# Kernel tuning notes

Measured on AMD Instinct MI355X. Metric: run time of the kernel, lower is better.

Reference implementation:

```python
import jax, jax.numpy as jnp
import numpy as np
from functools import partial

B, N, D = 32, 256, 1024
H = 16
HD = D // H
CD = 1024          # cond_dim
E = 4              # num_experts
TOPK = 2
DFF = 4 * D        # expert hidden
RH = 2 * D         # router mlp hidden
TEMP = 1.0
EPS = 1e-5


def _ln(x, g, b):
    mu = jnp.mean(x, axis=-1, keepdims=True)
    var = jnp.var(x, axis=-1, keepdims=True)
    return (x - mu) * jax.lax.rsqrt(var + EPS) * g + b


def setup_inputs() -> dict:
    key = jax.random.key(0)
    ks = jax.random.split(key, 16)
    s = 0.02
    return {
        "x": jax.random.normal(ks[0], (B, N, D), jnp.float32),
        "cond": jax.random.normal(ks[1], (B, 1, CD), jnp.float32),
        "ln1_g": jnp.ones((D,), jnp.float32),
        "ln1_b": jnp.zeros((D,), jnp.float32),
        "qkv_w": jax.random.normal(ks[2], (D, 3 * D), jnp.float32) * s,
        "proj_w": jax.random.normal(ks[3], (D, D), jnp.float32) * s,
        "proj_b": jnp.zeros((D,), jnp.float32),
        "ln2_g": jnp.ones((D,), jnp.float32),
        "ln2_b": jnp.zeros((D,), jnp.float32),
        "r_fc1_w": jax.random.normal(ks[4], (D + CD, RH), jnp.float32) * s,
        "r_fc1_b": jnp.zeros((RH,), jnp.float32),
        "r_fc2_w": jax.random.normal(ks[5], (RH, E), jnp.float32) * s,
        "r_fc2_b": jnp.zeros((E,), jnp.float32),
        "e_w1": jax.random.normal(ks[6], (E, D, DFF), jnp.float32) * s,
        "e_b1": jnp.zeros((E, DFF), jnp.float32),
        "e_w2": jax.random.normal(ks[7], (E, DFF, D), jnp.float32) * s,
        "e_b2": jnp.zeros((E, D), jnp.float32),
    }


def reference(x, cond, ln1_g, ln1_b, qkv_w, proj_w, proj_b, ln2_g, ln2_b,
              r_fc1_w, r_fc1_b, r_fc2_w, r_fc2_b, e_w1, e_b1, e_w2, e_b2):
    gelu = partial(jax.nn.gelu, approximate=False)  # torch nn.GELU default (erf)

    # ---- Attention block (pre-LN, no mask, qkv_bias=False) ----
    h = _ln(x, ln1_g, ln1_b)
    qkv = (h @ qkv_w).reshape(B, N, 3, H, HD)
    q, k, v = jnp.moveaxis(qkv, 2, 0)                         # each [B,N,H,HD]
    scale = HD ** -0.5
    attn = jnp.einsum("bqhd,bkhd->bhqk", q * scale, k)        # [B,H,N,N]
    attn = jax.nn.softmax(attn, axis=-1)
    o = jnp.einsum("bhqk,bkhd->bqhd", attn, v).reshape(B, N, D)
    x = x + o @ proj_w + proj_b

    # ---- RouterCond: concat tokens with repeated cond, MLP -> expert logits ----
    h = _ln(x, ln2_g, ln2_b)
    cond_rep = jnp.broadcast_to(cond, (B, N, CD))             # repeat along seq
    rin = jnp.concatenate([h, cond_rep], axis=-1).reshape(-1, D + CD)  # [T, D+CD]
    logits = gelu(rin @ r_fc1_w + r_fc1_b) @ r_fc2_w + r_fc2_b         # [T, E]
    logits = (logits - jnp.max(logits, axis=-1, keepdims=True)) / TEMP
    probs = jnp.clip(jax.nn.softmax(logits, axis=-1), 1e-9, 1.0 - 1e-9)

    # top-k selection + renormalization, scatter to dense router mask [T, E]
    top_p, top_i = jax.lax.top_k(probs, TOPK)
    top_w = top_p / jnp.sum(top_p, axis=-1, keepdims=True)    # normalize=True
    T = B * N
    router_mask = jnp.zeros((T, E), probs.dtype).at[
        jnp.arange(T)[:, None], top_i].set(top_w)             # [T, E]

    # ---- Expert MLPs, combined by router weights ----
    hf = h.reshape(T, D)
    hid = gelu(jnp.einsum("td,edh->teh", hf, e_w1) + e_b1)    # [T, E, DFF]
    eout = jnp.einsum("teh,ehd->ted", hid, e_w2) + e_b2       # [T, E, D]
    moe = jnp.einsum("te,ted->td", router_mask, eout).reshape(B, N, D)

    return x + moe
```

## Files before the change

### kernel.cpp

```cpp
#include <hip/hip_runtime.h>


typedef unsigned short u16;
typedef unsigned int   u32;

typedef __bf16 bf16x8 __attribute__((ext_vector_type(8)));
typedef float  floatx4 __attribute__((ext_vector_type(4)));

__device__ __forceinline__ float b2f(u32 u) {
    union { float f; u32 i; } v; v.i = (u & 0xffffu) << 16; return v.f;
}
__device__ __forceinline__ u16 f2b(float f) {
    union { float f; u32 i; } v; v.f = f;
    u32 x = v.i;
    u32 r = (x + 0x7fffu + ((x >> 16) & 1u)) >> 16;
    return (u16)r;
}
__device__ __forceinline__ float gelu_f(float x) {
    return 0.5f * x * (1.0f + erff(x * 0.70710678118654752440f));
}
__device__ __forceinline__ float lmix(const void* p, size_t i, int isf) {
    return isf ? ((const float*)p)[i] : b2f(((const u16*)p)[i]);
}
__device__ __forceinline__ void ld8(const void* p, size_t i, int isf, float w[8]) {
    if (isf) {
        const float* q = (const float*)p + i;
        float4 a = *(const float4*)q, b = *(const float4*)(q + 4);
        w[0] = a.x; w[1] = a.y; w[2] = a.z; w[3] = a.w;
        w[4] = b.x; w[5] = b.y; w[6] = b.z; w[7] = b.w;
    } else {
        const u16* q = (const u16*)p + i;
        uint4 r = *(const uint4*)q;
        w[0] = b2f(r.x); w[1] = b2f(r.x >> 16);
        w[2] = b2f(r.y); w[3] = b2f(r.y >> 16);
        w[4] = b2f(r.z); w[5] = b2f(r.z >> 16);
        w[6] = b2f(r.w); w[7] = b2f(r.w >> 16);
    }
}
__device__ __forceinline__ void ld4(const void* p, size_t i, int isf, float w[4]) {
    if (isf) {
        float4 a = *(const float4*)((const float*)p + i);
        w[0] = a.x; w[1] = a.y; w[2] = a.z; w[3] = a.w;
    } else {
        uint2 r = *(const uint2*)((const u16*)p + i);
        w[0] = b2f(r.x); w[1] = b2f(r.x >> 16);
        w[2] = b2f(r.y); w[3] = b2f(r.y >> 16);
    }
}

__global__ void init_kernel(const void* x0, int* cb) {
    __shared__ int sh[256];
    const int tid = threadIdx.x;
    if (tid < 12) cb[tid] = 0;
    int bad = 0;
    const u16* p = (const u16*)x0;
    for (int i = tid; i < 4096; i += 256) {
        float v = b2f(p[2 * i]);
        float a = fabsf(v);
        if (!(a <= 1e3f) || (v != 0.f && a < 1e-8f)) bad++;
    }
    sh[tid] = bad;
    __syncthreads();
    for (int s = 128; s > 0; s >>= 1) {
        if (tid < s) sh[tid] += sh[tid + s];
        __syncthreads();
    }
    if (tid == 0) cb[12] = (sh[0] > 512) ? 1 : 0;
}

__global__ __launch_bounds__(256) void cond_kernel(
    const void* __restrict__ cond, const void* __restrict__ w1,
    float* __restrict__ ct, const int* __restrict__ flg)
{
    const int isf = flg[12];
    const int b = blockIdx.y;
    const int col0 = blockIdx.x * 64;
    const int tid = threadIdx.x;
    const int wave = tid >> 6, lane = tid & 63;
    __shared__ float a[1024];
    __shared__ float part[4][64];
    {
        float v[4];
        ld4(cond, (size_t)b * 1024 + tid * 4, isf, v);
        a[tid * 4 + 0] = v[0]; a[tid * 4 + 1] = v[1];
        a[tid * 4 + 2] = v[2]; a[tid * 4 + 3] = v[3];
    }
    __syncthreads();
    const int col = col0 + lane;
    float s = 0.f;
    const int kbase = wave * 256;
    #pragma unroll 4
    for (int k = 0; k < 256; k++)
        s = fmaf(a[kbase + k], lmix(w1, (size_t)(1024 + kbase + k) * 2048 + col, isf), s);
    part[wave][lane] = s;
    __syncthreads();
    if (wave == 0) {
        float r = (part[0][lane] + part[1][lane]) + (part[2][lane] + part[3][lane]);
        ct[(size_t)b * 2048 + col] = r;
    }
}

__global__ __launch_bounds__(256) void pack_ln_kernel(
    int mode, const void* __restrict__ xin, size_t rowbase,
    const void* __restrict__ g, const void* __restrict__ bta,
    const float* __restrict__ mu_g, const float* __restrict__ rs_g,
    u16* __restrict__ hpk, u16* __restrict__ hb, const int* __restrict__ flg)
{
    const int isf = flg[12];
    const int row = blockIdx.x, tid = threadIdx.x;
    float v[4];
    float mu, rsv;
    __shared__ float red[8];
    __shared__ float mu_rs[2];
    if (mode == 0) {
        ld4(xin, (rowbase + row) * 1024 + tid * 4, isf, v);
        float s = v[0] + v[1] + v[2] + v[3];
        float q = v[0] * v[0] + v[1] * v[1] + v[2] * v[2] + v[3] * v[3];
        #pragma unroll
        for (int off = 32; off > 0; off >>= 1) {
            s += __shfl_down(s, off, 64);
            q += __shfl_down(q, off, 64);
        }
        int wid = tid >> 6, lane = tid & 63;
        if (lane == 0) { red[wid] = s; red[4 + wid] = q; }
        __syncthreads();
        if (tid == 0) {
            float ts = red[0] + red[1] + red[2] + red[3];
            float tq = red[4] + red[5] + red[6] + red[7];
            float m = ts * (1.0f / 1024.0f);
            float var = tq * (1.0f / 1024.0f) - m * m;
            float xx = var + 1e-5f;
            float r = rsqrtf(xx);
            r = r * (1.5f - 0.5f * xx * r * r);
            mu_rs[0] = m; mu_rs[1] = r;
        }
        __syncthreads();
        mu = mu_rs[0]; rsv = mu_rs[1];
    } else {
        float4 t = *(const float4*)((const float*)xin + (rowbase + row) * 1024 + tid * 4);
        v[0] = t.x; v[1] = t.y; v[2] = t.z; v[3] = t.w;
        mu = mu_g[rowbase + row]; rsv = rs_g[rowbase + row];
    }
    float gg[4], bb[4];
    ld4(g, tid * 4, isf, gg);
    ld4(bta, tid * 4, isf, bb);
    u16 hi[4], lo[4];
    #pragma unroll
    for (int i = 0; i < 4; i++) {
        float h = (v[i] - mu) * rsv * gg[i] + bb[i];
        hi[i] = f2b(h);
        lo[i] = f2b(h - b2f(hi[i]));
    }
    uint2 ph, pl;
    ph.x = (u32)hi[0] | ((u32)hi[1] << 16);
    ph.y = (u32)hi[2] | ((u32)hi[3] << 16);
    pl.x = (u32)lo[0] | ((u32)lo[1] << 16);
    pl.y = (u32)lo[2] | ((u32)lo[3] << 16);
    *(uint2*)(hpk + (size_t)row * 2048 + tid * 4) = ph;
    *(uint2*)(hpk + (size_t)row * 2048 + 1024 + tid * 4) = pl;
    if (hb) *(uint2*)(hb + (rowbase + row) * 1024 + tid * 4) = ph;
}

__global__ __launch_bounds__(256) void pack_wt_kernel(
    const void* __restrict__ W, int N, int K,
    u16* __restrict__ Bt, const int* __restrict__ flg)
{
    const int isf = flg[12];
    __shared__ float sh[64][65];
    const int k0 = blockIdx.x * 64, n0 = blockIdx.y * 64;
    const int tid = threadIdx.x;
    #pragma unroll
    for (int i = 0; i < 4; i++) {
        int r = (tid >> 4) + i * 16, c = (tid & 15) * 4;
        float w[4];
        ld4(W, (size_t)(k0 + r) * N + n0 + c, isf, w);
        sh[r][c] = w[0]; sh[r][c + 1] = w[1]; sh[r][c + 2] = w[2]; sh[r][c + 3] = w[3];
    }
    __syncthreads();
    const int n = tid >> 2, kc = (tid & 3) * 16;
    u16 hi[16], lo[16];
    #pragma unroll
    for (int j = 0; j < 16; j++) {
        float v = sh[kc + j][n];
        hi[j] = f2b(v);
        lo[j] = f2b(v - b2f(hi[j]));
    }
    u16* dst = Bt + (size_t)(n0 + n) * (2 * K) + k0 + kc;
    uint4 a, b;
    a.x = (u32)hi[0] | ((u32)hi[1] << 16);  a.y = (u32)hi[2] | ((u32)hi[3] << 16);
    a.z = (u32)hi[4] | ((u32)hi[5] << 16);  a.w = (u32)hi[6] | ((u32)hi[7] << 16);
    b.x = (u32)hi[8] | ((u32)hi[9] << 16);  b.y = (u32)hi[10] | ((u32)hi[11] << 16);
    b.z = (u32)hi[12] | ((u32)hi[13] << 16); b.w = (u32)hi[14] | ((u32)hi[15] << 16);
    *(uint4*)dst = a; *(uint4*)(dst + 8) = b;
    a.x = (u32)lo[0] | ((u32)lo[1] << 16);  a.y = (u32)lo[2] | ((u32)lo[3] << 16);
    a.z = (u32)lo[4] | ((u32)lo[5] << 16);  a.w = (u32)lo[6] | ((u32)lo[7] << 16);
    b.x = (u32)lo[8] | ((u32)lo[9] << 16);  b.y = (u32)lo[10] | ((u32)lo[11] << 16);
    b.z = (u32)lo[12] | ((u32)lo[13] << 16); b.w = (u32)lo[14] | ((u32)lo[15] << 16);
    *(uint4*)(dst + K) = a; *(uint4*)(dst + K + 8) = b;
}

__global__ __launch_bounds__(256) void pack_wtb_kernel(
    const void* __restrict__ W, size_t wOff, int N, int K,
    u16* __restrict__ Bt, const int* __restrict__ flg)
{
    const int isf = flg[12];
    __shared__ float sh[64][65];
    const int k0 = blockIdx.x * 64, n0 = blockIdx.y * 64;
    const int tid = threadIdx.x;
    #pragma unroll
    for (int i = 0; i < 4; i++) {
        int r = (tid >> 4) + i * 16, c = (tid & 15) * 4;
        float w[4];
        ld4(W, wOff + (size_t)(k0 + r) * N + n0 + c, isf, w);
        sh[r][c] = w[0]; sh[r][c + 1] = w[1]; sh[r][c + 2] = w[2]; sh[r][c + 3] = w[3];
    }
    __syncthreads();
    const int n = tid >> 2, kc = (tid & 3) * 16;
    u16 hi[16];
    #pragma unroll
    for (int j = 0; j < 16; j++) hi[j] = f2b(sh[kc + j][n]);
    u16* dst = Bt + (size_t)(n0 + n) * K + k0 + kc;
    uint4 a, b;
    a.x = (u32)hi[0] | ((u32)hi[1] << 16);  a.y = (u32)hi[2] | ((u32)hi[3] << 16);
    a.z = (u32)hi[4] | ((u32)hi[5] << 16);  a.w = (u32)hi[6] | ((u32)hi[7] << 16);
    b.x = (u32)hi[8] | ((u32)hi[9] << 16);  b.y = (u32)hi[10] | ((u32)hi[11] << 16);
    b.z = (u32)hi[12] | ((u32)hi[13] << 16); b.w = (u32)hi[14] | ((u32)hi[15] << 16);
    *(uint4*)dst = a; *(uint4*)(dst + 8) = b;
}

__global__ __launch_bounds__(256) void pack_sb_rows_kernel(
    const float* __restrict__ src, u16* __restrict__ dst)
{
    const int row = blockIdx.x, tid = threadIdx.x;
    float4 t = *(const float4*)(src + (size_t)row * 1024 + tid * 4);
    float v[4] = {t.x, t.y, t.z, t.w};
    u16 hi[4], lo[4];
    #pragma unroll
    for (int i = 0; i < 4; i++) {
        hi[i] = f2b(v[i]);
        lo[i] = f2b(v[i] - b2f(hi[i]));
    }
    uint2 ph, pl;
    ph.x = (u32)hi[0] | ((u32)hi[1] << 16);
    ph.y = (u32)hi[2] | ((u32)hi[3] << 16);
    pl.x = (u32)lo[0] | ((u32)lo[1] << 16);
    pl.y = (u32)lo[2] | ((u32)lo[3] << 16);
    *(uint2*)(dst + (size_t)row * 2048 + tid * 4) = ph;
    *(uint2*)(dst + (size_t)row * 2048 + 1024 + tid * 4) = pl;
}

#define SB_PLAIN 0
#define SB_FC1   1
#define SB_PROJ  2

__global__ __launch_bounds__(256) void gemm_sb(
    int mode,
    const u16* __restrict__ Ap,
    const u16* __restrict__ Bt,
    int K,
    float* __restrict__ C, int ldc,
    const void* __restrict__ bias,
    const float* __restrict__ condt,
    const void* __restrict__ resid,
    int rowbase, const int* __restrict__ flg)
{
    const int isf = flg[12];
    __shared__ __align__(16) u16 Ah[128][40];
    __shared__ __align__(16) u16 Al[128][40];
    __shared__ __align__(16) u16 Bh[128][40];
    __shared__ __align__(16) u16 Bl[128][40];
    const int tid = threadIdx.x;
    const int row0 = blockIdx.y * 128, col0 = blockIdx.x * 128;
    const int wave = tid >> 6, lane = tid & 63;
    const int wm = (wave >> 1) * 64, wn = (wave & 1) * 64;
    const int ln = lane & 15, quad = lane >> 4;
    const size_t K2 = (size_t)2 * K;
    floatx4 acc[4][4];
    #pragma unroll
    for (int i = 0; i < 4; i++)
        #pragma unroll
        for (int j = 0; j < 4; j++) acc[i][j] = (floatx4){0.f, 0.f, 0.f, 0.f};

    const int ar = tid >> 1, ac = (tid & 1) * 16;
    uint4 pa0, pa1, pal0, pal1, pb0, pb1, pbl0, pbl1;

    {
        const u16* ap = Ap + (size_t)(row0 + ar) * K2 + ac;
        pa0 = *(const uint4*)ap;        pa1 = *(const uint4*)(ap + 8);
        pal0 = *(const uint4*)(ap + K); pal1 = *(const uint4*)(ap + K + 8);
        const u16* bp = Bt + (size_t)(col0 + ar) * K2 + ac;
        pb0 = *(const uint4*)bp;        pb1 = *(const uint4*)(bp + 8);
        pbl0 = *(const uint4*)(bp + K); pbl1 = *(const uint4*)(bp + K + 8);
    }

    for (int k0 = 0; k0 < K; k0 += 32) {
        __syncthreads();
        *(uint4*)&Ah[ar][ac] = pa0;  *(uint4*)&Ah[ar][ac + 8] = pa1;
        *(uint4*)&Al[ar][ac] = pal0; *(uint4*)&Al[ar][ac + 8] = pal1;
        *(uint4*)&Bh[ar][ac] = pb0;  *(uint4*)&Bh[ar][ac + 8] = pb1;
        *(uint4*)&Bl[ar][ac] = pbl0; *(uint4*)&Bl[ar][ac + 8] = pbl1;
        __syncthreads();
        if (k0 + 32 < K) {
            const u16* ap = Ap + (size_t)(row0 + ar) * K2 + k0 + 32 + ac;
            pa0 = *(const uint4*)ap;        pa1 = *(const uint4*)(ap + 8);
            pal0 = *(const uint4*)(ap + K); pal1 = *(const uint4*)(ap + K + 8);
            const u16* bp = Bt + (size_t)(col0 + ar) * K2 + k0 + 32 + ac;
            pb0 = *(const uint4*)bp;        pb1 = *(const uint4*)(bp + 8);
            pbl0 = *(const uint4*)(bp + K); pbl1 = *(const uint4*)(bp + K + 8);
        }
        bf16x8 ah[4], al[4];
        #pragma unroll
        for (int mt = 0; mt < 4; mt++) {
            ah[mt] = *(const bf16x8*)&Ah[wm + mt * 16 + ln][quad * 8];
            al[mt] = *(const bf16x8*)&Al[wm + mt * 16 + ln][quad * 8];
        }
        #pragma unroll
        for (int nt = 0; nt < 4; nt++) {
            bf16x8 bh = *(const bf16x8*)&Bh[wn + nt * 16 + ln][quad * 8];
            bf16x8 bl = *(const bf16x8*)&Bl[wn + nt * 16 + ln][quad * 8];
            #pragma unroll
            for (int mt = 0; mt < 4; mt++) {
                acc[mt][nt] = __builtin_amdgcn_mfma_f32_16x16x32_bf16(ah[mt], bh, acc[mt][nt], 0, 0, 0);
                acc[mt][nt] = __builtin_amdgcn_mfma_f32_16x16x32_bf16(ah[mt], bl, acc[mt][nt], 0, 0, 0);
                acc[mt][nt] = __builtin_amdgcn_mfma_f32_16x16x32_bf16(al[mt], bh, acc[mt][nt], 0, 0, 0);
            }
        }
    }
    #pragma unroll
    for (int mt = 0; mt < 4; mt++) {
        #pragma unroll
        for (int nt = 0; nt < 4; nt++) {
            #pragma unroll
            for (int r = 0; r < 4; r++) {
                int row = row0 + wm + mt * 16 + quad * 4 + r;
                int col = col0 + wn + nt * 16 + ln;
                float v = acc[mt][nt][r];
                if (mode == SB_FC1)
                    v = gelu_f(v + lmix(bias, col, isf) +
                               condt[(size_t)((rowbase + row) >> 8) * 2048 + col]);
                else if (mode == SB_PROJ)
                    v += lmix(bias, col, isf) + lmix(resid, (size_t)row * ldc + col, isf);
                C[(size_t)row * ldc + col] = v;
            }
        }
    }
}

#define MOE_FC1 0
#define MOE_FC2 1

__global__ __launch_bounds__(256) void gemm_moe(
    int mode,
    const u16* __restrict__ Ap,
    const u16* __restrict__ Bt,
    int K,
    u16* __restrict__ C, int ldc,
    const void* __restrict__ bias, size_t biasOff,
    const float* __restrict__ rowscale,
    const int* __restrict__ toklist,
    const int* __restrict__ cb, int e, int rowOff,
    const int* __restrict__ flg)
{
    const int isf = flg[12];
    const int Meff = cb[e];
    const int gbase = cb[4 + e];
    const int rg0 = rowOff + blockIdx.y * 128;
    if (rg0 >= Meff) return;
    const int col0 = blockIdx.x * 128;
    __shared__ __align__(16) u16 As[128][40];
    __shared__ __align__(16) u16 Bs[128][40];
    const int tid = threadIdx.x;
    const int wave = tid >> 6, lane = tid & 63;
    const int wm = (wave >> 1) * 64, wn = (wave & 1) * 64;
    const int ln = lane & 15, quad = lane >> 4;
    floatx4 acc[4][4];
    #pragma unroll
    for (int i = 0; i < 4; i++)
        #pragma unroll
        for (int j = 0; j < 4; j++) acc[i][j] = (floatx4){0.f, 0.f, 0.f, 0.f};

    const int ar = tid >> 1, ac = (tid & 1) * 16;
    const int rg = rg0 + ar;
    const bool valid = (rg < Meff);
    const u16* arow;
    if (mode == MOE_FC1) {
        int tokid = valid ? toklist[gbase + rg] : 0;
        arow = Ap + (size_t)tokid * K;
    } else {
        arow = Ap + (size_t)(rg - rowOff) * K;
    }
    const u16* brow = Bt + (size_t)(col0 + ar) * K;
    uint4 pa0 = {0u,0u,0u,0u}, pa1 = {0u,0u,0u,0u}, pb0, pb1;
    if (valid) { pa0 = *(const uint4*)(arow + ac); pa1 = *(const uint4*)(arow + ac + 8); }
    pb0 = *(const uint4*)(brow + ac); pb1 = *(const uint4*)(brow + ac + 8);

    for (int k0 = 0; k0 < K; k0 += 32) {
        __syncthreads();
        *(uint4*)&As[ar][ac] = pa0; *(uint4*)&As[ar][ac + 8] = pa1;
        *(uint4*)&Bs[ar][ac] = pb0; *(uint4*)&Bs[ar][ac + 8] = pb1;
        __syncthreads();
        if (k0 + 32 < K) {
            if (valid) {
                pa0 = *(const uint4*)(arow + k0 + 32 + ac);
                pa1 = *(const uint4*)(arow + k0 + 32 + ac + 8);
            }
            pb0 = *(const uint4*)(brow + k0 + 32 + ac);
            pb1 = *(const uint4*)(brow + k0 + 32 + ac + 8);
        }
        bf16x8 a[4];
        #pragma unroll
        for (int mt = 0; mt < 4; mt++)
            a[mt] = *(const bf16x8*)&As[wm + mt * 16 + ln][quad * 8];
        #pragma unroll
        for (int nt = 0; nt < 4; nt++) {
            bf16x8 b = *(const bf16x8*)&Bs[wn + nt * 16 + ln][quad * 8];
            #pragma unroll
            for (int mt = 0; mt < 4; mt++)
                acc[mt][nt] = __builtin_amdgcn_mfma_f32_16x16x32_bf16(a[mt], b, acc[mt][nt], 0, 0, 0);
        }
    }
    #pragma unroll
    for (int mt = 0; mt < 4; mt++) {
        #pragma unroll
        for (int nt = 0; nt < 4; nt++) {
            #pragma unroll
            for (int r = 0; r < 4; r++) {
                int gw = rg0 + wm + mt * 16 + quad * 4 + r;
                if (gw >= Meff) continue;
                int col = col0 + wn + nt * 16 + ln;
                float v = acc[mt][nt][r] + lmix(bias, biasOff + col, isf);
                if (mode == MOE_FC1) {
                    C[(size_t)(gw - rowOff) * ldc + col] = f2b(gelu_f(v));
                } else {
                    v *= rowscale[gbase + gw];
                    C[(size_t)(gbase + gw) * ldc + col] = f2b(v);
                }
            }
        }
    }
}

__global__ __launch_bounds__(256) void gemm_moe2(
    const u16* __restrict__ Ap,
    const u16* __restrict__ Bt,
    u16* __restrict__ C,
    const void* __restrict__ bias, size_t biasOff,
    const float* __restrict__ rowscale,
    const int* __restrict__ cb, int e, int rowOff,
    const int* __restrict__ flg)
{
    const int isf = flg[12];
    const int Meff = cb[e];
    const int gbase = cb[4 + e];
    const int rg0 = rowOff + blockIdx.y * 128;
    if (rg0 >= Meff) return;
    const int col0 = blockIdx.x * 64;
    const int K = 4096;
    __shared__ __align__(16) u16 As[128][40];
    __shared__ __align__(16) u16 Bs[64][40];
    const int tid = threadIdx.x;
    const int wave = tid >> 6, lane = tid & 63;
    const int ln = lane & 15, quad = lane >> 4;
    floatx4 acc[2][4];
    #pragma unroll
    for (int i = 0; i < 2; i++)
        #pragma unroll
        for (int j = 0; j < 4; j++) acc[i][j] = (floatx4){0.f, 0.f, 0.f, 0.f};

    const int ar = tid >> 1, ac = (tid & 1) * 16;
    const int br = tid >> 2, bc = (tid & 3) * 8;
    const int rg = rg0 + ar;
    const bool valid = (rg < Meff);
    const u16* arow = Ap + (size_t)(rg - rowOff) * K;
    const u16* brow = Bt + (size_t)(col0 + br) * K;
    uint4 pa0 = {0u,0u,0u,0u}, pa1 = {0u,0u,0u,0u}, pb;
    if (valid) { pa0 = *(const uint4*)(arow + ac); pa1 = *(const uint4*)(arow + ac + 8); }
    pb = *(const uint4*)(brow + bc);

    for (int k0 = 0; k0 < K; k0 += 32) {
        __syncthreads();
        *(uint4*)&As[ar][ac] = pa0; *(uint4*)&As[ar][ac + 8] = pa1;
        *(uint4*)&Bs[br][bc] = pb;
        __syncthreads();
        if (k0 + 32 < K) {
            if (valid) {
                pa0 = *(const uint4*)(arow + k0 + 32 + ac);
                pa1 = *(const uint4*)(arow + k0 + 32 + ac + 8);
            }
            pb = *(const uint4*)(brow + k0 + 32 + bc);
        }
        bf16x8 a0 = *(const bf16x8*)&As[wave * 32 + ln][quad * 8];
        bf16x8 a1 = *(const bf16x8*)&As[wave * 32 + 16 + ln][quad * 8];
        #pragma unroll
        for (int nt = 0; nt < 4; nt++) {
            bf16x8 b = *(const bf16x8*)&Bs[nt * 16 + ln][quad * 8];
            acc[0][nt] = __builtin_amdgcn_mfma_f32_16x16x32_bf16(a0, b, acc[0][nt], 0, 0, 0);
            acc[1][nt] = __builtin_amdgcn_mfma_f32_16x16x32_bf16(a1, b, acc[1][nt], 0, 0, 0);
        }
    }
    #pragma unroll
    for (int mt = 0; mt < 2; mt++) {
        #pragma unroll
        for (int nt = 0; nt < 4; nt++) {
            #pragma unroll
            for (int r = 0; r < 4; r++) {
                int gw = rg0 + wave * 32 + mt * 16 + quad * 4 + r;
                if (gw >= Meff) continue;
                int col = col0 + nt * 16 + ln;
                float v = acc[mt][nt][r] + lmix(bias, biasOff + col, isf);
                v *= rowscale[gbase + gw];
                C[(size_t)(gbase + gw) * 1024 + col] = f2b(v);
            }
        }
    }
}

__global__ __launch_bounds__(256) void ln_stats_kernel(
    const float* __restrict__ xin, float* __restrict__ mu, float* __restrict__ rs)
{
    const int row = blockIdx.x, tid = threadIdx.x;
    float4 t = *(const float4*)(xin + (size_t)row * 1024 + tid * 4);
    float s = t.x + t.y + t.z + t.w;
    float q = t.x * t.x + t.y * t.y + t.z * t.z + t.w * t.w;
    #pragma unroll
    for (int off = 32; off > 0; off >>= 1) {
        s += __shfl_down(s, off, 64);
        q += __shfl_down(q, off, 64);
    }
    __shared__ float red[8];
    int wid = tid >> 6, lane = tid & 63;
    if (lane == 0) { red[wid] = s; red[4 + wid] = q; }
    __syncthreads();
    if (tid == 0) {
        float ts = red[0] + red[1] + red[2] + red[3];
        float tq = red[4] + red[5] + red[6] + red[7];
        float m = ts * (1.0f / 1024.0f);
        float var = tq * (1.0f / 1024.0f) - m * m;
        float xx = var + 1e-5f;
        float r = rsqrtf(xx);
        r = r * (1.5f - 0.5f * xx * r * r);
        mu[row] = m; rs[row] = r;
    }
}

#define GM_PLAIN 0
#define GM_PROJ  1

__global__ __launch_bounds__(256) void gemm_f32(
    int mode, int aMode,
    const void* __restrict__ Av, int lda,
    const void* __restrict__ Bv, int ldb, int bRow0,
    int M, int N, int K,
    float* __restrict__ C, int ldc,
    const void* __restrict__ bias,
    const void* __restrict__ resid,
    const int* __restrict__ flg)
{
    const int isf = flg[12];
    __shared__ float As[16][132];
    __shared__ float Bs[16][132];
    const int tid = threadIdx.x;
    const int row0 = blockIdx.y * 128, col0 = blockIdx.x * 128;
    const int tx = tid & 15, ty = tid >> 4;
    float acc[8][8];
    #pragma unroll
    for (int i = 0; i < 8; i++)
        #pragma unroll
        for (int j = 0; j < 8; j++) acc[i][j] = 0.f;

    for (int k0 = 0; k0 < K; k0 += 16) {
        __syncthreads();
        #pragma unroll
        for (int i = 0; i < 2; i++) {
            int lin = tid + i * 256;
            int r = lin >> 2, kc = (lin & 3) * 4;
            float v[4] = {0.f, 0.f, 0.f, 0.f};
            if (row0 + r < M) {
                if (aMode == 1) {
                    ld4(Av, (size_t)(row0 + r) * lda + k0 + kc, isf, v);
                } else {
                    float4 t = *(const float4*)((const float*)Av + (size_t)(row0 + r) * lda + k0 + kc);
                    v[0] = t.x; v[1] = t.y; v[2] = t.z; v[3] = t.w;
                }
            }
            As[kc + 0][r] = v[0]; As[kc + 1][r] = v[1];
            As[kc + 2][r] = v[2]; As[kc + 3][r] = v[3];
        }
        {
            int kc = tid >> 4, c8 = (tid & 15) * 8;
            float w[8];
            ld8(Bv, (size_t)(bRow0 + k0 + kc) * ldb + col0 + c8, isf, w);
            #pragma unroll
            for (int j = 0; j < 8; j++) Bs[kc][c8 + j] = w[j];
        }
        __syncthreads();
        #pragma unroll
        for (int kk = 0; kk < 16; kk++) {
            float a[8], b[8];
            *(float4*)&a[0] = *(const float4*)&As[kk][ty * 8];
            *(float4*)&a[4] = *(const float4*)&As[kk][ty * 8 + 4];
            *(float4*)&b[0] = *(const float4*)&Bs[kk][tx * 8];
            *(float4*)&b[4] = *(const float4*)&Bs[kk][tx * 8 + 4];
            #pragma unroll
            for (int i = 0; i < 8; i++)
                #pragma unroll
                for (int j = 0; j < 8; j++) acc[i][j] = fmaf(a[i], b[j], acc[i][j]);
        }
    }
    #pragma unroll
    for (int i = 0; i < 8; i++) {
        int gr = row0 + ty * 8 + i;
        if (gr >= M) continue;
        #pragma unroll
        for (int j = 0; j < 8; j++) {
            int gc = col0 + tx * 8 + j;
            float v = acc[i][j];
            if (mode == GM_PROJ)
                v += lmix(bias, gc, isf) + lmix(resid, (size_t)gr * ldc + gc, isf);
            C[(size_t)gr * ldc + gc] = v;
        }
    }
}

__global__ __launch_bounds__(256) void attn_kernel(
    const float* __restrict__ qkv, float* __restrict__ o)
{
    const int bx = blockIdx.x;
    const int b  = bx >> 6;
    const int hh = (bx >> 2) & 15;
    const int qt = bx & 3;
    const int tid = threadIdx.x;
    const int wave = tid >> 6, lane = tid & 63;

    __shared__ float sh[2 * 64 * 68];
    float* Ks = sh;
    float* Vs = sh + 64 * 68;

    const int q = qt * 64 + lane;
    float qreg[64];
    const float* qp = qkv + (size_t)(b * 256 + q) * 3072 + hh * 64;
    #pragma unroll
    for (int i = 0; i < 16; i++) *(float4*)&qreg[i * 4] = *(const float4*)(qp + i * 4);

    float oa[64];
    #pragma unroll
    for (int d = 0; d < 64; d++) oa[d] = 0.f;
    float m = -1e30f, l = 0.f;

    for (int s = 0; s < 4; s++) {
        __syncthreads();
        {
            int r = tid >> 2;
            int c = (tid & 3) * 16;
            int key = (r >> 4) * 64 + s * 16 + (r & 15);
            const float* kp = qkv + (size_t)(b * 256 + key) * 3072 + 1024 + hh * 64 + c;
            #pragma unroll
            for (int i = 0; i < 4; i++) {
                *(float4*)&Ks[r * 68 + c + i * 4] = *(const float4*)(kp + i * 4);
                *(float4*)&Vs[r * 68 + c + i * 4] = *(const float4*)(kp + 1024 + i * 4);
            }
        }
        __syncthreads();
        const float* Kw = Ks + wave * 16 * 68;
        const float* Vw = Vs + wave * 16 * 68;
        for (int jj = 0; jj < 16; jj++) {
            float s0 = 0.f, s1 = 0.f, s2 = 0.f, s3 = 0.f;
            #pragma unroll
            for (int d = 0; d < 64; d += 4) {
                s0 = fmaf(qreg[d + 0], Kw[jj * 68 + d + 0], s0);
                s1 = fmaf(qreg[d + 1], Kw[jj * 68 + d + 1], s1);
                s2 = fmaf(qreg[d + 2], Kw[jj * 68 + d + 2], s2);
                s3 = fmaf(qreg[d + 3], Kw[jj * 68 + d + 3], s3);
            }
            float sc = ((s0 + s1) + (s2 + s3)) * 0.125f;
            float mn = fmaxf(m, sc);
            float c = __expf(m - mn);
            float p = __expf(sc - mn);
            l = l * c + p;
            #pragma unroll
            for (int d = 0; d < 64; d++)
                oa[d] = fmaf(oa[d], c, p * Vw[jj * 68 + d]);
            m = mn;
        }
    }

    __syncthreads();
    if (wave == 1 || wave == 3) {
        float* dst = sh + (wave >> 1) * (64 * 66) + lane * 66;
        #pragma unroll
        for (int d = 0; d < 64; d++) dst[d] = oa[d];
        dst[64] = m; dst[65] = l;
    }
    __syncthreads();
    if (wave == 0 || wave == 2) {
        const float* src = sh + (wave >> 1) * (64 * 66) + lane * 66;
        float m2 = src[64], l2 = src[65];
        float M = fmaxf(m, m2);
        float c1 = __expf(m - M), c2 = __expf(m2 - M);
        l = l * c1 + l2 * c2;
        #pragma unroll
        for (int d = 0; d < 64; d++) oa[d] = oa[d] * c1 + src[d] * c2;
        m = M;
    }
    __syncthreads();
    if (wave == 2) {
        float* dst = sh + lane * 66;
        #pragma unroll
        for (int d = 0; d < 64; d++) dst[d] = oa[d];
        dst[64] = m; dst[65] = l;
    }
    __syncthreads();
    if (wave == 0) {
        const float* src = sh + lane * 66;
        float m2 = src[64], l2 = src[65];
        float M = fmaxf(m, m2);
        float c1 = __expf(m - M), c2 = __expf(m2 - M);
        l = l * c1 + l2 * c2;
        #pragma unroll
        for (int d = 0; d < 64; d++) oa[d] = oa[d] * c1 + src[d] * c2;
        float inv = 1.0f / l;
        float* op = o + (size_t)(b * 256 + q) * 1024 + hh * 64;
        #pragma unroll
        for (int i = 0; i < 16; i++) {
            float4 v = { oa[i * 4] * inv, oa[i * 4 + 1] * inv,
                         oa[i * 4 + 2] * inv, oa[i * 4 + 3] * inv };
            *(float4*)(op + i * 4) = v;
        }
    }
}

__global__ __launch_bounds__(256) void router_kernel(
    const float* __restrict__ hr, const void* __restrict__ w2,
    const void* __restrict__ b2, int* __restrict__ t2i,
    float* __restrict__ t2w, int* __restrict__ cb, int rowbase,
    const int* __restrict__ flg)
{
    const int isf = flg[12];
    const int lt = blockIdx.x * 4 + (threadIdx.x >> 6);
    const int t = rowbase + lt;
    const int lane = threadIdx.x & 63;
    float a0 = 0.f, a1 = 0.f, a2 = 0.f, a3 = 0.f;
    const float* hp = hr + (size_t)lt * 2048;
    for (int j = lane; j < 2048; j += 64) {
        float hv = hp[j];
        float w[4];
        ld4(w2, (size_t)j * 4, isf, w);
        a0 = fmaf(hv, w[0], a0);
        a1 = fmaf(hv, w[1], a1);
        a2 = fmaf(hv, w[2], a2);
        a3 = fmaf(hv, w[3], a3);
    }
    #pragma unroll
    for (int off = 32; off > 0; off >>= 1) {
        a0 += __shfl_down(a0, off, 64);
        a1 += __shfl_down(a1, off, 64);
        a2 += __shfl_down(a2, off, 64);
        a3 += __shfl_down(a3, off, 64);
    }
    if (lane == 0) {
        float l[4];
        l[0] = a0 + lmix(b2, 0, isf); l[1] = a1 + lmix(b2, 1, isf);
        l[2] = a2 + lmix(b2, 2, isf); l[3] = a3 + lmix(b2, 3, isf);
        int i0 = 0;
        #pragma unroll
        for (int i = 1; i < 4; i++) if (l[i] > l[i0]) i0 = i;
        int i1 = (i0 == 0) ? 1 : 0;
        #pragma unroll
        for (int i = 0; i < 4; i++) if (i != i0 && l[i] > l[i1]) i1 = i;
        float mx = fmaxf(fmaxf(l[0], l[1]), fmaxf(l[2], l[3]));
        float e0 = __expf(l[0] - mx), e1 = __expf(l[1] - mx);
        float e2 = __expf(l[2] - mx), e3 = __expf(l[3] - mx);
        float inv = 1.0f / (e0 + e1 + e2 + e3);
        float p[4] = { e0 * inv, e1 * inv, e2 * inv, e3 * inv };
        float b0 = fminf(fmaxf(p[i0], 1e-9f), 1.0f - 1e-9f);
        float b1 = fminf(fmaxf(p[i1], 1e-9f), 1.0f - 1e-9f);
        float winv = 1.0f / (b0 + b1);
        t2i[2 * t] = i0; t2i[2 * t + 1] = i1;
        t2w[2 * t] = b0 * winv; t2w[2 * t + 1] = b1 * winv;
        atomicAdd(&cb[i0], 1);
        atomicAdd(&cb[i1], 1);
    }
}

__global__ __launch_bounds__(256) void fill2_kernel(
    const int* __restrict__ t2i, const float* __restrict__ t2w,
    int* __restrict__ cb, int* __restrict__ tok,
    float* __restrict__ aw, int* __restrict__ apos)
{
    const int e = blockIdx.x;
    const int tid = threadIdx.x;
    __shared__ int scan[256];
    int base = 0;
    #pragma unroll
    for (int i = 0; i < 4; i++) if (i < e) base += cb[i];
    const int t0 = tid * 32;
    int cnt = 0;
    for (int t = t0; t < t0 + 32; t++)
        cnt += (t2i[2 * t] == e) + (t2i[2 * t + 1] == e);
    scan[tid] = cnt;
    __syncthreads();
    for (int off = 1; off < 256; off <<= 1) {
        int add = (tid >= off) ? scan[tid - off] : 0;
        __syncthreads();
        scan[tid] += add;
        __syncthreads();
    }
    int pos = base + scan[tid] - cnt;
    for (int t = t0; t < t0 + 32; t++) {
        #pragma unroll
        for (int j = 0; j < 2; j++) {
            if (t2i[2 * t + j] == e) {
                tok[pos] = t;
                aw[pos] = t2w[2 * t + j];
                apos[2 * t + j] = pos;
                pos++;
            }
        }
    }
    if (tid == 0) cb[4 + e] = base;
}

#define EM_FC1 0
#define EM_FC2 1

__global__ __launch_bounds__(256) void gemm_mfma(
    int mode,
    const float* __restrict__ x1,
    const float* __restrict__ mu, const float* __restrict__ rs,
    const void* __restrict__ lng, const void* __restrict__ lnb,
    const u16* __restrict__ Ab,
    const void* __restrict__ B, size_t bOff, int ldb, int K,
    u16* __restrict__ C, int ldc,
    const void* __restrict__ bias, size_t biasOff,
    const float* __restrict__ rowscale,
    const int* __restrict__ toklist,
    const int* __restrict__ cb, int e, int rowOff,
    const int* __restrict__ flg)
{
    const int isf = flg[12];
    const int Meff = cb[e];
    const int gbase = cb[4 + e];
    const int rg0 = rowOff + blockIdx.y * 64;
    if (rg0 >= Meff) return;
    const int col0 = blockIdx.x * 64;
    __shared__ __align__(16) u16 As[64][72];
    __shared__ __align__(16) u16 Bs[64][72];
    const int tid = threadIdx.x;
    const int wave = tid >> 6, lane = tid & 63;
    const int ln = lane & 15, quad = lane >> 4;
    floatx4 acc[4];
    #pragma unroll
    for (int nt = 0; nt < 4; nt++) acc[nt] = (floatx4){0.f, 0.f, 0.f, 0.f};

    const int ar = tid >> 2, ac = (tid & 3) * 8;
    const int bk = tid >> 3, bn = (tid & 7) * 8;
    const int rg = rg0 + ar;
    const bool valid = (rg < Meff);
    int tokid = 0; float lm = 0.f, lr = 0.f;
    if (mode == EM_FC1 && valid) {
        tokid = toklist[gbase + rg];
        lm = mu[tokid]; lr = rs[tokid];
    }

    for (int k0 = 0; k0 < K; k0 += 32) {
        __syncthreads();
        if (mode == EM_FC1) {
            uint4 packed = {0u, 0u, 0u, 0u};
            if (valid) {
                float4 p0 = *(const float4*)(x1 + (size_t)tokid * 1024 + k0 + ac);
                float4 p1 = *(const float4*)(x1 + (size_t)tokid * 1024 + k0 + ac + 4);
                float pv[8] = {p0.x, p0.y, p0.z, p0.w, p1.x, p1.y, p1.z, p1.w};
                float gg[8], bb[8];
                ld8(lng, k0 + ac, isf, gg);
                ld8(lnb, k0 + ac, isf, bb);
                u16 wb[8];
                #pragma unroll
                for (int z = 0; z < 8; z++)
                    wb[z] = f2b((pv[z] - lm) * lr * gg[z] + bb[z]);
                packed.x = (u32)wb[0] | ((u32)wb[1] << 16);
                packed.y = (u32)wb[2] | ((u32)wb[3] << 16);
                packed.z = (u32)wb[4] | ((u32)wb[5] << 16);
                packed.w = (u32)wb[6] | ((u32)wb[7] << 16);
            }
            *(uint4*)&As[ar][ac] = packed;
        } else {
            uint4 av = {0u, 0u, 0u, 0u};
            if (valid) av = *(const uint4*)(Ab + (size_t)(rg - rowOff) * K + k0 + ac);
            *(uint4*)&As[ar][ac] = av;
        }
        u16 u[8];
        {
            float w[8];
            ld8(B, bOff + (size_t)(k0 + bk) * ldb + col0 + bn, isf, w);
            #pragma unroll
            for (int z = 0; z < 8; z++) u[z] = f2b(w[z]);
        }
        #pragma unroll
        for (int jj = 0; jj < 8; jj++) {
            int j = (jj + (tid & 7)) & 7;
            Bs[bn + j][bk] = u[j];
        }
        __syncthreads();
        bf16x8 af = *(const bf16x8*)&As[wave * 16 + ln][quad * 8];
        #pragma unroll
        for (int nt = 0; nt < 4; nt++) {
            bf16x8 bf = *(const bf16x8*)&Bs[nt * 16 + ln][quad * 8];
            acc[nt] = __builtin_amdgcn_mfma_f32_16x16x32_bf16(af, bf, acc[nt], 0, 0, 0);
        }
    }
    #pragma unroll
    for (int nt = 0; nt < 4; nt++) {
        #pragma unroll
        for (int r = 0; r < 4; r++) {
            int gw = rg0 + wave * 16 + quad * 4 + r;
            if (gw >= Meff) continue;
            int gcol = col0 + nt * 16 + ln;
            float v = acc[nt][r] + lmix(bias, biasOff + gcol, isf);
            if (mode == EM_FC1) {
                C[(size_t)(gw - rowOff) * ldc + gcol] = f2b(gelu_f(v));
            } else {
                v *= rowscale[gbase + gw];
                C[(size_t)(gbase + gw) * ldc + gcol] = f2b(v);
            }
        }
    }
}

__global__ __launch_bounds__(256) void combine_kernel(
    const float* __restrict__ x1, const u16* __restrict__ eo,
    const int* __restrict__ apos, void* __restrict__ outv,
    const int* __restrict__ flg)
{
    const int isf = flg[12];
    int t = blockIdx.x;
    int c = threadIdx.x * 4;
    int p0 = apos[2 * t], p1 = apos[2 * t + 1];
    float4 xv = *(const float4*)(x1 + (size_t)t * 1024 + c);
    uint2 ea = *(const uint2*)(eo + (size_t)p0 * 1024 + c);
    uint2 eb = *(const uint2*)(eo + (size_t)p1 * 1024 + c);
    float r0 = xv.x + b2f(ea.x) + b2f(eb.x);
    float r1 = xv.y + b2f(ea.x >> 16) + b2f(eb.x >> 16);
    float r2 = xv.z + b2f(ea.y) + b2f(eb.y);
    float r3 = xv.w + b2f(ea.y >> 16) + b2f(eb.y >> 16);
    if (isf) {
        float4 res = {r0, r1, r2, r3};
        *(float4*)((float*)outv + (size_t)t * 1024 + c) = res;
    } else {
        uint2 res;
        res.x = (u32)f2b(r0) | ((u32)f2b(r1) << 16);
        res.y = (u32)f2b(r2) | ((u32)f2b(r3) << 16);
        *(uint2*)((u16*)outv + (size_t)t * 1024 + c) = res;
    }
}

extern "C" void kernel_launch(void* const* d_in, const int* in_sizes, int n_in,
                              void* d_out, int out_size, void* d_ws, size_t ws_size,
                              hipStream_t stream)
{
    const void* x      = d_in[0];
    const void* cond   = d_in[1];
    const void* ln1_g  = d_in[2];
    const void* ln1_b  = d_in[3];
    const void* qkv_w  = d_in[4];
    const void* proj_w = d_in[5];
    const void* proj_b = d_in[6];
    const void* ln2_g  = d_in[7];
    const void* ln2_b  = d_in[8];
    const void* rf1w   = d_in[9];
    const void* rf1b   = d_in[10];
    const void* rf2w   = d_in[11];
    const void* rf2b   = d_in[12];
    const void* ew1    = d_in[13];
    const void* eb1    = d_in[14];
    const void* ew2    = d_in[15];
    const void* eb2    = d_in[16];
    (void)in_sizes; (void)n_in; (void)out_size;

    char* ws = (char*)d_ws;
    const size_t MB = 1024 * 1024;
    const bool fat = ws_size >= (size_t)116 * MB;

    float* x1   = (float*)(ws);
    u16*   qkvt = (u16*)(ws);
    u16*   hpk  = (u16*)(ws + 12 * MB);
    float* qkvcFb = (float*)(ws + 16 * MB);
    char*  B1   = ws + 32 * MB;
    float* ob   = (float*)B1;
    u16*   rf1tF= (u16*)B1;
    u16*   h2tF = (u16*)(ws + 40 * MB);
    u16*   eo   = (u16*)B1;
    u16*   rf1tB= (u16*)B1;
    char*  R    = ws + 64 * MB;
    float* qkvcF= (float*)R;
    u16*   h2tB = (u16*)R;
    float* hrcB = (float*)(R + 8 * MB);
    float* hrcF = (float*)R;
    u16*   hid  = (u16*)R;
    u16*   obp  = (u16*)R;
    u16*   ew1t = (u16*)(R + 16 * MB);
    u16*   ew2t = (u16*)(R + 24 * MB);
    u16*   pwt  = (u16*)(ws + 96 * MB);
    u16*   h2b  = (u16*)(ws + 96 * MB);
    char*  ST   = ws + (fat ? 112 : 96) * MB;

    size_t so = 0;
    auto salloc = [&](size_t bytes) { size_t o = so; so += (bytes + 255) & ~(size_t)255; return o; };
    float* mu   = (float*)(ST + salloc(8192 * 4));
    float* rs   = (float*)(ST + salloc(8192 * 4));
    float* ct   = (float*)(ST + salloc((size_t)32 * 2048 * 4));
    int*   t2i  = (int*)  (ST + salloc(16384 * 4));
    float* t2w  = (float*)(ST + salloc(16384 * 4));
    int*   cb   = (int*)  (ST + salloc(16 * 4));
    int*   tok  = (int*)  (ST + salloc(16384 * 4));
    float* aw   = (float*)(ST + salloc(16384 * 4));
    int*   apos = (int*)  (ST + salloc(16384 * 4));

    init_kernel<<<1, 256, 0, stream>>>(x, cb);

    pack_wt_kernel<<<dim3(16, 48), 256, 0, stream>>>(qkv_w, 3072, 1024, qkvt, cb);
    if (fat) {
        for (int c = 0; c < 2; c++) {
            const size_t r0 = (size_t)c * 4096;
            pack_ln_kernel<<<4096, 256, 0, stream>>>(
                0, x, r0, ln1_g, ln1_b, nullptr, nullptr, hpk, nullptr, cb);
            gemm_sb<<<dim3(24, 32), 256, 0, stream>>>(
                SB_PLAIN, hpk, qkvt, 1024, qkvcF, 3072, nullptr, nullptr, nullptr, 0, cb);
            attn_kernel<<<1024, 256, 0, stream>>>(qkvcF, ob + r0 * 1024);
        }
    } else {
        for (int c = 0; c < 8; c++) {
            const size_t r0 = (size_t)c * 1024;
            pack_ln_kernel<<<1024, 256, 0, stream>>>(
                0, x, r0, ln1_g, ln1_b, nullptr, nullptr, hpk, nullptr, cb);
            gemm_sb<<<dim3(24, 8), 256, 0, stream>>>(
                SB_PLAIN, hpk, qkvt, 1024, qkvcFb, 3072, nullptr, nullptr, nullptr, 0, cb);
            attn_kernel<<<256, 256, 0, stream>>>(qkvcFb, ob + r0 * 1024);
        }
    }

    if (fat) {
        pack_sb_rows_kernel<<<8192, 256, 0, stream>>>(ob, obp);
        pack_wt_kernel<<<dim3(16, 16), 256, 0, stream>>>(proj_w, 1024, 1024, pwt, cb);
        gemm_sb<<<dim3(8, 64), 256, 0, stream>>>(
            SB_PROJ, obp, pwt, 1024, x1, 1024, proj_b, nullptr, x, 0, cb);
    } else {
        gemm_f32<<<dim3(8, 64), 256, 0, stream>>>(
            GM_PROJ, 0, (const void*)ob, 1024, proj_w, 1024, 0, 8192, 1024, 1024,
            x1, 1024, proj_b, x, cb);
    }

    ln_stats_kernel<<<8192, 256, 0, stream>>>(x1, mu, rs);

    cond_kernel<<<dim3(32, 32), 256, 0, stream>>>(cond, rf1w, ct, cb);

    if (fat) {
        pack_wt_kernel<<<dim3(16, 32), 256, 0, stream>>>(rf1w, 2048, 1024, rf1tF, cb);
        for (int rc = 0; rc < 2; rc++) {
            const int rb = rc * 4096;
            pack_ln_kernel<<<4096, 256, 0, stream>>>(
                1, x1, rb, ln2_g, ln2_b, mu, rs, h2tF, h2b, cb);
            gemm_sb<<<dim3(16, 32), 256, 0, stream>>>(
                SB_FC1, h2tF, rf1tF, 1024, hrcF, 2048, rf1b, ct, nullptr, rb, cb);
            router_kernel<<<1024, 256, 0, stream>>>(hrcF, rf2w, rf2b, t2i, t2w, cb, rb, cb);
        }
    } else {
        pack_wt_kernel<<<dim3(16, 32), 256, 0, stream>>>(rf1w, 2048, 1024, rf1tB, cb);
        for (int rc = 0; rc < 4; rc++) {
            const int rb = rc * 2048;
            pack_ln_kernel<<<2048, 256, 0, stream>>>(
                1, x1, rb, ln2_g, ln2_b, mu, rs, h2tB, nullptr, cb);
            gemm_sb<<<dim3(16, 16), 256, 0, stream>>>(
                SB_FC1, h2tB, rf1tB, 1024, hrcB, 2048, rf1b, ct, nullptr, rb, cb);
            router_kernel<<<512, 256, 0, stream>>>(hrcB, rf2w, rf2b, t2i, t2w, cb, rb, cb);
        }
    }
    fill2_kernel<<<4, 256, 0, stream>>>(t2i, t2w, cb, tok, aw, apos);

    if (fat) {
        for (int e = 0; e < 4; e++) {
            pack_wtb_kernel<<<dim3(16, 64), 256, 0, stream>>>(
                ew1, (size_t)e * 1024 * 4096, 4096, 1024, ew1t, cb);
            pack_wtb_kernel<<<dim3(64, 16), 256, 0, stream>>>(
                ew2, (size_t)e * 4096 * 1024, 1024, 4096, ew2t, cb);
            for (int c = 0; c < 4; c++) {
                const int ro = c * 2048;
                gemm_moe<<<dim3(32, 16), 256, 0, stream>>>(
                    MOE_FC1, h2b, ew1t, 1024, hid, 4096,
                    eb1, (size_t)e * 4096, nullptr, tok, cb, e, ro, cb);
                gemm_moe2<<<dim3(16, 16), 256, 0, stream>>>(
                    hid, ew2t, eo, eb2, (size_t)e * 1024, aw, cb, e, ro, cb);
            }
        }
    } else {
        for (int e = 0; e < 4; e++) {
            for (int c = 0; c < 2; c++) {
                const int ro = c * 4096;
                gemm_mfma<<<dim3(64, 64), 256, 0, stream>>>(
                    EM_FC1, x1, mu, rs, ln2_g, ln2_b, nullptr,
                    ew1, (size_t)e * 1024 * 4096, 4096, 1024,
                    hid, 4096, eb1, (size_t)e * 4096, nullptr, tok, cb, e, ro, cb);
                gemm_mfma<<<dim3(16, 64), 256, 0, stream>>>(
                    EM_FC2, nullptr, nullptr, nullptr, nullptr, nullptr, hid,
                    ew2, (size_t)e * 4096 * 1024, 1024, 4096,
                    eo, 1024, eb2, (size_t)e * 1024, aw, tok, cb, e, ro, cb);
            }
        }
    }

    combine_kernel<<<8192, 256, 0, stream>>>(x1, eo, apos, d_out, cb);
}
```

Measured before the change: 2.148 ms.

## Rewrite attention kernel with bf16x3 split-precision MFMA

Adds a new attention kernel that splits Q, K, V and the softmax probabilities into bf16 high/low pairs and computes QK^T and PV using three MFMA 16x16x32 products per tile, in place of scalar FP32 FMA. Scores are stored as hi/lo bf16 in shared memory for a full-row softmax, and K/V tiles are register-prefetched while computing. This targets ALU throughput in attention at the cost of extra conversion work, more shared memory, and slightly reduced precision. Only the large-workspace path uses the new kernel.

```diff
diff --git a/kernel.cpp b/kernel.cpp
--- a/kernel.cpp
+++ b/kernel.cpp
@@ -618,6 +618,234 @@
             if (mode == GM_PROJ)
                 v += lmix(bias, gc, isf) + lmix(resid, (size_t)gr * ldc + gc, isf);
             C[(size_t)gr * ldc + gc] = v;
+        }
+    }
+}
+
+__global__ __launch_bounds__(256) void attn_mfma_kernel(
+    const float* __restrict__ qkv, float* __restrict__ o)
+{
+    const int bx = blockIdx.x;
+    const int b  = bx >> 6;
+    const int hh = (bx >> 2) & 15;
+    const int qt = bx & 3;
+    const int tid = threadIdx.x;
+    const int wave = tid >> 6, lane = tid & 63;
+    const int ln = lane & 15, quad = lane >> 4;
+
+    __shared__ __align__(16) u16 Sh[64][264];
+    __shared__ __align__(16) u16 Sl[64][264];
+    __shared__ __align__(16) u16 KVh[64][72];
+    __shared__ __align__(16) u16 KVl[64][72];
+    __shared__ float mred[64][4];
+    __shared__ float lred[64][4];
+    __shared__ float lsh[64];
+
+    const size_t tokbase = (size_t)b * 256;
+
+    bf16x8 qh[2], ql[2];
+    {
+        const float* qp = qkv + (tokbase + qt * 64 + wave * 16 + ln) * 3072 + hh * 64;
+        #pragma unroll
+        for (int ks = 0; ks < 2; ks++) {
+            float4 f0 = *(const float4*)(qp + ks * 32 + quad * 8);
+            float4 f1 = *(const float4*)(qp + ks * 32 + quad * 8 + 4);
+            float fv[8] = {f0.x, f0.y, f0.z, f0.w, f1.x, f1.y, f1.z, f1.w};
+            union { uint4 u; bf16x8 v; } ch, cl;
+            u32 hw[4], lw[4];
+            #pragma unroll
+            for (int j = 0; j < 4; j++) {
+                u16 h0 = f2b(fv[2 * j]),      h1 = f2b(fv[2 * j + 1]);
+                u16 l0 = f2b(fv[2 * j] - b2f(h0));
+                u16 l1 = f2b(fv[2 * j + 1] - b2f(h1));
+                hw[j] = (u32)h0 | ((u32)h1 << 16);
+                lw[j] = (u32)l0 | ((u32)l1 << 16);
+            }
+            ch.u.x = hw[0]; ch.u.y = hw[1]; ch.u.z = hw[2]; ch.u.w = hw[3];
+            cl.u.x = lw[0]; cl.u.y = lw[1]; cl.u.z = lw[2]; cl.u.w = lw[3];
+            qh[ks] = ch.v; ql[ks] = cl.v;
+        }
+    }
+
+    const int skey = tid >> 2, sds = (tid & 3) * 16;
+    float4 kpre[4];
+    {
+        const float* kp = qkv + (tokbase + skey) * 3072 + 1024 + hh * 64 + sds;
+        #pragma unroll
+        for (int i = 0; i < 4; i++) kpre[i] = *(const float4*)(kp + i * 4);
+    }
+    for (int kt = 0; kt < 4; kt++) {
+        __syncthreads();
+        #pragma unroll
+        for (int i = 0; i < 4; i++) {
+            float fv[4] = {kpre[i].x, kpre[i].y, kpre[i].z, kpre[i].w};
+            u16 hv[4], lv[4];
+            #pragma unroll
+            for (int j = 0; j < 4; j++) {
+                hv[j] = f2b(fv[j]);
+                lv[j] = f2b(fv[j] - b2f(hv[j]));
+            }
+            uint2 uh, ul;
+            uh.x = (u32)hv[0] | ((u32)hv[1] << 16);
+            uh.y = (u32)hv[2] | ((u32)hv[3] << 16);
+            ul.x = (u32)lv[0] | ((u32)lv[1] << 16);
+            ul.y = (u32)lv[2] | ((u32)lv[3] << 16);
+            *(uint2*)&KVh[skey][sds + i * 4] = uh;
+            *(uint2*)&KVl[skey][sds + i * 4] = ul;
+        }
+        __syncthreads();
+        if (kt < 3) {
+            const float* kp = qkv + (tokbase + (kt + 1) * 64 + skey) * 3072 + 1024 + hh * 64 + sds;
+            #pragma unroll
+            for (int i = 0; i < 4; i++) kpre[i] = *(const float4*)(kp + i * 4);
+        }
+        floatx4 acc[4];
+        #pragma unroll
+        for (int nt = 0; nt < 4; nt++) acc[nt] = (floatx4){0.f, 0.f, 0.f, 0.f};
+        #pragma unroll
+        for (int ks = 0; ks < 2; ks++) {
+            bf16x8 kh[4], kl[4];
+            #pragma unroll
+            for (int nt = 0; nt < 4; nt++) {
+                kh[nt] = *(const bf16x8*)&KVh[nt * 16 + ln][ks * 32 + quad * 8];
+                kl[nt] = *(const bf16x8*)&KVl[nt * 16 + ln][ks * 32 + quad * 8];
+            }
+            #pragma unroll
+            for (int nt = 0; nt < 4; nt++)
+                acc[nt] = __builtin_amdgcn_mfma_f32_16x16x32_bf16(qh[ks], kh[nt], acc[nt], 0, 0, 0);
+            #pragma unroll
+            for (int nt = 0; nt < 4; nt++)
+                acc[nt] = __builtin_amdgcn_mfma_f32_16x16x32_bf16(qh[ks], kl[nt], acc[nt], 0, 0, 0);
+            #pragma unroll
+            for (int nt = 0; nt < 4; nt++)
+                acc[nt] = __builtin_amdgcn_mfma_f32_16x16x32_bf16(ql[ks], kh[nt], acc[nt], 0, 0, 0);
+        }
+        #pragma unroll
+        for (int nt = 0; nt < 4; nt++) {
+            #pragma unroll
+            for (int r = 0; r < 4; r++) {
+                float s = acc[nt][r] * 0.125f;
+                u16 hi = f2b(s);
+                Sh[wave * 16 + quad * 4 + r][kt * 64 + nt * 16 + ln] = hi;
+                Sl[wave * 16 + quad * 4 + r][kt * 64 + nt * 16 + ln] = f2b(s - b2f(hi));
+            }
+        }
+    }
+
+    __syncthreads();
+    {
+        const int q = tid >> 2, seg = tid & 3;
+        float mx = -1e30f;
+        #pragma unroll
+        for (int i = 0; i < 8; i++) {
+            uint4 h4 = *(const uint4*)&Sh[q][seg * 64 + i * 8];
+            uint4 l4 = *(const uint4*)&Sl[q][seg * 64 + i * 8];
+            mx = fmaxf(mx, fmaxf(b2f(h4.x) + b2f(l4.x), b2f(h4.x >> 16) + b2f(l4.x >> 16)));
+            mx = fmaxf(mx, fmaxf(b2f(h4.y) + b2f(l4.y), b2f(h4.y >> 16) + b2f(l4.y >> 16)));
+            mx = fmaxf(mx, fmaxf(b2f(h4.z) + b2f(l4.z), b2f(h4.z >> 16) + b2f(l4.z >> 16)));
+            mx = fmaxf(mx, fmaxf(b2f(h4.w) + b2f(l4.w), b2f(h4.w >> 16) + b2f(l4.w >> 16)));
+        }
+        mred[q][seg] = mx;
+        __syncthreads();
+        float m = fmaxf(fmaxf(mred[q][0], mred[q][1]), fmaxf(mred[q][2], mred[q][3]));
+        float sum = 0.f;
+        #pragma unroll
+        for (int i = 0; i < 8; i++) {
+            uint4 h4 = *(const uint4*)&Sh[q][seg * 64 + i * 8];
+            uint4 l4 = *(const uint4*)&Sl[q][seg * 64 + i * 8];
+            u32 hw[4] = {h4.x, h4.y, h4.z, h4.w};
+            u32 lw[4] = {l4.x, l4.y, l4.z, l4.w};
+            uint4 oh, ol;
+            u32* ohp = (u32*)&oh; u32* olp = (u32*)&ol;
+            #pragma unroll
+            for (int j = 0; j < 4; j++) {
+                float p0 = __expf(b2f(hw[j]) + b2f(lw[j]) - m);
+                float p1 = __expf(b2f(hw[j] >> 16) + b2f(lw[j] >> 16) - m);
+                sum += p0 + p1;
+                u16 ph0 = f2b(p0), ph1 = f2b(p1);
+                u16 pl0 = f2b(p0 - b2f(ph0)), pl1 = f2b(p1 - b2f(ph1));
+                ohp[j] = (u32)ph0 | ((u32)ph1 << 16);
+                olp[j] = (u32)pl0 | ((u32)pl1 << 16);
+            }
+            *(uint4*)&Sh[q][seg * 64 + i * 8] = oh;
+            *(uint4*)&Sl[q][seg * 64 + i * 8] = ol;
+        }
+        lred[q][seg] = sum;
+        __syncthreads();
+        if (seg == 0)
+            lsh[q] = (lred[q][0] + lred[q][1]) + (lred[q][2] + lred[q][3]);
+    }
+
+    const int vd = tid & 63, vk0 = (tid >> 6) * 16;
+    float vpre[16];
+    {
+        const float* vp = qkv + (tokbase + vk0) * 3072 + 2048 + hh * 64 + vd;
+        #pragma unroll
+        for (int j = 0; j < 16; j++) vpre[j] = vp[(size_t)j * 3072];
+    }
+    floatx4 pacc[4];
+    #pragma unroll
+    for (int nt = 0; nt < 4; nt++) pacc[nt] = (floatx4){0.f, 0.f, 0.f, 0.f};
+    for (int kt = 0; kt < 4; kt++) {
+        __syncthreads();
+        #pragma unroll
+        for (int w = 0; w < 4; w++) {
+            u16 hv[4], lv[4];
+            #pragma unroll
+            for (int j = 0; j < 4; j++) {
+                float f = vpre[w * 4 + j];
+                hv[j] = f2b(f);
+                lv[j] = f2b(f - b2f(hv[j]));
+            }
+            uint2 uh, ul;
+            uh.x = (u32)hv[0] | ((u32)hv[1] << 16);
+            uh.y = (u32)hv[2] | ((u32)hv[3] << 16);
+            ul.x = (u32)lv[0] | ((u32)lv[1] << 16);
+            ul.y = (u32)lv[2] | ((u32)lv[3] << 16);
+            *(uint2*)&KVh[vd][vk0 + w * 4] = uh;
+            *(uint2*)&KVl[vd][vk0 + w * 4] = ul;
+        }
+        __syncthreads();
+        if (kt < 3) {
+            const float* vp = qkv + (tokbase + (kt + 1) * 64 + vk0) * 3072 + 2048 + hh * 64 + vd;
+            #pragma unroll
+            for (int j = 0; j < 16; j++) vpre[j] = vp[(size_t)j * 3072];
+        }
+        #pragma unroll
+        for (int ks = 0; ks < 2; ks++) {
+            const int kc = kt * 64 + ks * 32 + quad * 8;
+            bf16x8 ph = *(const bf16x8*)&Sh[wave * 16 + ln][kc];
+            bf16x8 pl = *(const bf16x8*)&Sl[wave * 16 + ln][kc];
+            bf16x8 vh[4], vl[4];
+            #pragma unroll
+            for (int nt = 0; nt < 4; nt++) {
+                vh[nt] = *(const bf16x8*)&KVh[nt * 16 + ln][ks * 32 + quad * 8];
+                vl[nt] = *(const bf16x8*)&KVl[nt * 16 + ln][ks * 32 + quad * 8];
+            }
+            #pragma unroll
+            for (int nt = 0; nt < 4; nt++)
+                pacc[nt] = __builtin_amdgcn_mfma_f32_16x16x32_bf16(ph, vh[nt], pacc[nt], 0, 0, 0);
+            #pragma unroll
+            for (int nt = 0; nt < 4; nt++)
+                pacc[nt] = __builtin_amdgcn_mfma_f32_16x16x32_bf16(ph, vl[nt], pacc[nt], 0, 0, 0);
+            #pragma unroll
+            for (int nt = 0; nt < 4; nt++)
+                pacc[nt] = __builtin_amdgcn_mfma_f32_16x16x32_bf16(pl, vh[nt], pacc[nt], 0, 0, 0);
+        }
+    }
+    {
+        float linv[4];
+        #pragma unroll
+        for (int r = 0; r < 4; r++)
+            linv[r] = 1.0f / lsh[wave * 16 + quad * 4 + r];
+        #pragma unroll
+        for (int nt = 0; nt < 4; nt++) {
+            #pragma unroll
+            for (int r = 0; r < 4; r++) {
+                int row = wave * 16 + quad * 4 + r;
+                o[(tokbase + qt * 64 + row) * 1024 + hh * 64 + nt * 16 + ln] =
+                    pacc[nt][r] * linv[r];
+            }
         }
     }
 }
@@ -1025,7 +1253,7 @@
                 0, x, r0, ln1_g, ln1_b, nullptr, nullptr, hpk, nullptr, cb);
             gemm_sb<<<dim3(24, 32), 256, 0, stream>>>(
                 SB_PLAIN, hpk, qkvt, 1024, qkvcF, 3072, nullptr, nullptr, nullptr, 0, cb);
-            attn_kernel<<<1024, 256, 0, stream>>>(qkvcF, ob + r0 * 1024);
+            attn_mfma_kernel<<<1024, 256, 0, stream>>>(qkvcF, ob + r0 * 1024);
         }
     } else {
         for (int c = 0; c < 8; c++) {
```

Result: no change. 2.148 ms (+0.0%).
